# Optimization experiments

Hardware: AMD Instinct MI355X
Metric: run time of the kernel (lower is better)

Reference implementation:

```python
import jax, jax.numpy as jnp
import numpy as np

MAX_THRESHOLD = 0.95


def leaky_clamp(x, lo, hi, slope):
    # identity inside [lo, hi], linear with `slope` outside
    return jnp.where(x < lo, lo + slope * (x - lo),
                     jnp.where(x > hi, hi + slope * (x - hi), x))


def or_gate_layer(x, W, tau_adder):
    # x: (B, in), W: (out, in)
    in_f = W.shape[1]
    tau_floor = float(np.log(in_f - 1) + np.log(MAX_THRESHOLD) - np.log(1.0 - MAX_THRESHOLD))
    tau = tau_floor + jax.nn.leaky_relu(tau_adder, negative_slope=0.05)
    aw = leaky_clamp(W, 0.0, 1.0, 0.1)           # (out, in)
    z = x[:, None, :] * aw[None, :, :]           # (B, out, in) broadcast
    p = jax.nn.softmax(tau * z, axis=-1)         # tau-scaled softmax over in
    return jnp.sum(p * z, axis=-1)               # (B, out)


def setup_inputs() -> dict:
    key = jax.random.key(0)
    ks = jax.random.split(key, 9)
    input_dim = 512
    layer_dims = [1024, 512, 256, 128]
    x = jax.random.uniform(ks[0], (128, input_dim), dtype=jnp.float32)
    in_dim = input_dim * 2
    out = {"x": x}
    for i, out_dim in enumerate(layer_dims):
        out[f"W{i}"] = jax.random.normal(ks[1 + i], (out_dim, in_dim), dtype=jnp.float32)
        out[f"tau{i}"] = jnp.zeros((), dtype=jnp.float32)
        in_dim = out_dim  # only_inverter=True
    return out


def reference(x, W0, W1, W2, W3, tau0, tau1, tau2, tau3):
    h = jnp.concatenate([x, 1.0 - x], axis=-1)   # pass_invert
    for W, t in ((W0, tau0), (W1, tau1), (W2, tau2), (W3, tau3)):
        h = 1.0 - or_gate_layer(h, W, t)         # only_inverter: invert after every layer
    return h
```

## Files before the change

### kernel.cpp

```cpp
#include <hip/hip_runtime.h>
#include <math.h>

#if defined(__has_builtin)
#  if __has_builtin(__builtin_amdgcn_exp2f)
#    define EXP2F(x) __builtin_amdgcn_exp2f(x)
#  endif
#endif
#ifndef EXP2F
#  define EXP2F(x) __expf(0.69314718055994530942f * (x))
#endif

__device__ __forceinline__ float fast_exp2(float x) {
  const float M = 12582912.0f;
  const float y = x + M;
  const float n = y - M;
  const float f = x - n;
  float p = fmaf(f, 0.055504109f, 0.24022651f);
  p = fmaf(f, p, 0.69314718f);
  p = fmaf(f, p, 1.0f);
  const int r = (__float_as_int(y) << 23) + __float_as_int(p);
  return __int_as_float(r);
}

template <int IN, int OUT, int BB, bool FIRST>
__launch_bounds__(256, 4)
__global__ void or_layer(const float* __restrict__ hin,
                         const float* __restrict__ W,
                         const float* __restrict__ tau_ptr,
                         float* __restrict__ hout,
                         float tau_floor) {
  constexpr int OBB = 2;
  constexpr int NIT = IN / 64;
  constexpr int nOT = OUT / 32;
  constexpr int IN4 = IN / 4;

  __shared__ float4 lds_h[BB][IN4];

  const int tid  = threadIdx.x;
  const int lane = tid & 63;
  const int wid  = tid >> 6;
  const int il   = lane & 15;
  const int og   = lane >> 4;

  const int ot = blockIdx.x % nOT;
  const int bt = blockIdx.x / nOT;
  const int b0 = bt * BB;
  const int o0 = ot * 32 + wid * 8 + og * OBB;

  const float ta  = tau_ptr[0];
  const float tau = tau_floor + (ta >= 0.0f ? ta : 0.05f * ta);
  const float c2  = tau * 1.44269504088896340736f;

  const float4* __restrict__ Wv = (const float4*)W;
  const float4* __restrict__ Hv = (const float4*)hin;

  if (FIRST) {
    constexpr int HALF4 = IN / 8;
    for (int idx = tid; idx < BB * HALF4; idx += 256) {
      const int r = idx / HALF4;
      const int k = idx - r * HALF4;
      const float4 v = Hv[(b0 + r) * HALF4 + k];
      lds_h[r][k] = v;
      lds_h[r][HALF4 + k] =
          make_float4(1.0f - v.x, 1.0f - v.y, 1.0f - v.z, 1.0f - v.w);
    }
  } else {
    for (int idx = tid; idx < BB * IN4; idx += 256) {
      const int r = idx / IN4;
      const int k = idx - r * IN4;
      lds_h[r][k] = Hv[(b0 + r) * IN4 + k];
    }
  }
  __syncthreads();

  float s[BB][OBB], t[BB][OBB];
#pragma unroll
  for (int r = 0; r < BB; ++r)
#pragma unroll
    for (int c = 0; c < OBB; ++c) { s[r][c] = 0.0f; t[r][c] = 0.0f; }

  const float4* wp0 = Wv + (size_t)(o0 + 0) * IN4 + il;
  const float4* wp1 = Wv + (size_t)(o0 + 1) * IN4 + il;

  float4 wcur0 = wp0[0];
  float4 wcur1 = wp1[0];

#pragma unroll 2
  for (int ic = 0; ic < NIT; ++ic) {
    const int icn = (ic + 1 < NIT) ? (ic + 1) : (NIT - 1);
    const float4 wnxt0 = wp0[icn * 16];
    const float4 wnxt1 = wp1[icn * 16];

    float hc[BB][4];
#pragma unroll
    for (int r = 0; r < BB; ++r) {
      const float4 v = lds_h[r][ic * 16 + il];
      hc[r][0] = v.x; hc[r][1] = v.y; hc[r][2] = v.z; hc[r][3] = v.w;
    }

    float cw[OBB][4];
    {
      const float wj0[4] = {wcur0.x, wcur0.y, wcur0.z, wcur0.w};
      const float wj1[4] = {wcur1.x, wcur1.y, wcur1.z, wcur1.w};
#pragma unroll
      for (int j = 0; j < 4; ++j) {
        float m  = fminf(fmaxf(wj0[j], 0.0f), 1.0f);
        cw[0][j] = c2 * fmaf(0.1f, wj0[j] - m, m);
        m        = fminf(fmaxf(wj1[j], 0.0f), 1.0f);
        cw[1][j] = c2 * fmaf(0.1f, wj1[j] - m, m);
      }
    }

#pragma unroll
    for (int r = 0; r < BB; ++r)
#pragma unroll
      for (int c = 0; c < OBB; ++c)
#pragma unroll
        for (int j = 0; j < 4; ++j) {
          const float arg = cw[c][j] * hc[r][j];
          const float e = (j & 1) ? fast_exp2(arg) : EXP2F(arg);
          s[r][c] += e;
          t[r][c]  = fmaf(arg, e, t[r][c]);
        }

    wcur0 = wnxt0;
    wcur1 = wnxt1;
  }

#pragma unroll
  for (int m = 1; m < 16; m <<= 1)
#pragma unroll
    for (int r = 0; r < BB; ++r)
#pragma unroll
      for (int c = 0; c < OBB; ++c) {
        s[r][c] += __shfl_xor(s[r][c], m, 64);
        t[r][c] += __shfl_xor(t[r][c], m, 64);
      }

  if (il == 0) {
    const float inv_c2 = 1.0f / c2;
#pragma unroll
    for (int r = 0; r < BB; ++r)
#pragma unroll
      for (int c = 0; c < OBB; ++c) {
        const float out = t[r][c] / s[r][c] * inv_c2;
        hout[(b0 + r) * OUT + (o0 + c)] = 1.0f - out;
      }
  }
}

extern "C" void kernel_launch(void* const* d_in, const int* in_sizes, int n_in,
                              void* d_out, int out_size, void* d_ws, size_t ws_size,
                              hipStream_t stream) {
  const float* x    = (const float*)d_in[0];
  const float* W0   = (const float*)d_in[1];
  const float* tau0 = (const float*)d_in[2];
  const float* W1   = (const float*)d_in[3];
  const float* tau1 = (const float*)d_in[4];
  const float* W2   = (const float*)d_in[5];
  const float* tau2 = (const float*)d_in[6];
  const float* W3   = (const float*)d_in[7];
  const float* tau3 = (const float*)d_in[8];

  float* h1  = (float*)d_ws;
  float* h2  = h1 + 128 * 1024;
  float* h3  = h2 + 128 * 512;
  float* out = (float*)d_out;

  const double LOGR = 2.9444389791664403;
  const float tf1024 = (float)(log(1023.0) + LOGR);
  const float tf512  = (float)(log(511.0)  + LOGR);
  const float tf256  = (float)(log(255.0)  + LOGR);

  or_layer<1024, 1024, 4, true ><<<1024, 256, 0, stream>>>(x,  W0, tau0, h1,  tf1024);
  or_layer<1024,  512, 2, false><<<1024, 256, 0, stream>>>(h1, W1, tau1, h2,  tf1024);
  or_layer< 512,  256, 1, false><<<1024, 256, 0, stream>>>(h2, W2, tau2, h3,  tf512);
  or_layer< 256,  128, 1, false><<< 512, 256, 0, stream>>>(h3, W3, tau3, out, tf256);
}
```

Before: 123.8 us.

## Fuse four OR-gate layers into one persistent cooperative kernel with grid syncs

Replaces four separate layer launches with a single cooperative persistent kernel. It loops over tiles per layer and puts grid-wide syncs between layers, with a fallback to the separate launches if the cooperative launch fails. This targets launch overhead and the tail gaps between dependent kernels. In exchange it adds grid barrier costs and grid-stride tile scheduling. It also uses a fixed 16KB shared buffer sized for the largest layer, which may lower occupancy for the smaller layers.

```diff
diff --git a/kernel.cpp b/kernel.cpp
--- a/kernel.cpp
+++ b/kernel.cpp
@@ -1,5 +1,8 @@
 #include <hip/hip_runtime.h>
+#include <hip/hip_cooperative_groups.h>
 #include <math.h>
+
+namespace cg = cooperative_groups;
 
 #if defined(__has_builtin)
 #  if __has_builtin(__builtin_amdgcn_exp2f)
@@ -23,130 +26,166 @@
 }
 
 template <int IN, int OUT, int BB, bool FIRST>
+__device__ __forceinline__ void layer_body(const float* __restrict__ hin,
+                                           const float* __restrict__ W,
+                                           const float* __restrict__ tau_ptr,
+                                           float* __restrict__ hout,
+                                           float tau_floor,
+                                           float4* __restrict__ lds_h) {
+  constexpr int OBB = 2;
+  constexpr int NIT = IN / 64;
+  constexpr int nOT = OUT / 32;
+  constexpr int IN4 = IN / 4;
+  constexpr int TILES = nOT * (128 / BB);
+
+  const int tid  = threadIdx.x;
+  const int lane = tid & 63;
+  const int wid  = tid >> 6;
+  const int il   = lane & 15;
+  const int og   = lane >> 4;
+
+  const float ta  = tau_ptr[0];
+  const float tau = tau_floor + (ta >= 0.0f ? ta : 0.05f * ta);
+  const float c2  = tau * 1.44269504088896340736f;
+  const float inv_c2 = 1.0f / c2;
+
+  const float4* __restrict__ Wv = (const float4*)W;
+  const float4* __restrict__ Hv = (const float4*)hin;
+
+  for (int tile = blockIdx.x; tile < TILES; tile += gridDim.x) {
+    const int ot = tile % nOT;
+    const int bt = tile / nOT;
+    const int b0 = bt * BB;
+    const int o0 = ot * 32 + wid * 8 + og * OBB;
+
+    __syncthreads();
+    if (FIRST) {
+      constexpr int HALF4 = IN / 8;
+      for (int idx = tid; idx < BB * HALF4; idx += 256) {
+        const int r = idx / HALF4;
+        const int k = idx - r * HALF4;
+        const float4 v = Hv[(b0 + r) * HALF4 + k];
+        lds_h[r * IN4 + k] = v;
+        lds_h[r * IN4 + HALF4 + k] =
+            make_float4(1.0f - v.x, 1.0f - v.y, 1.0f - v.z, 1.0f - v.w);
+      }
+    } else {
+      for (int idx = tid; idx < BB * IN4; idx += 256) {
+        const int r = idx / IN4;
+        const int k = idx - r * IN4;
+        lds_h[r * IN4 + k] = Hv[(b0 + r) * IN4 + k];
+      }
+    }
+    __syncthreads();
+
+    float s[BB][OBB], t[BB][OBB];
+#pragma unroll
+    for (int r = 0; r < BB; ++r)
+#pragma unroll
+      for (int c = 0; c < OBB; ++c) { s[r][c] = 0.0f; t[r][c] = 0.0f; }
+
+    const float4* wp0 = Wv + (size_t)(o0 + 0) * IN4 + il;
+    const float4* wp1 = Wv + (size_t)(o0 + 1) * IN4 + il;
+    float4 wcur0 = wp0[0];
+    float4 wcur1 = wp1[0];
+
+#pragma unroll 2
+    for (int ic = 0; ic < NIT; ++ic) {
+      const int icn = (ic + 1 < NIT) ? (ic + 1) : (NIT - 1);
+      const float4 wnxt0 = wp0[icn * 16];
+      const float4 wnxt1 = wp1[icn * 16];
+
+      float hc[BB][4];
+#pragma unroll
+      for (int r = 0; r < BB; ++r) {
+        const float4 v = lds_h[r * IN4 + ic * 16 + il];
+        hc[r][0] = v.x; hc[r][1] = v.y; hc[r][2] = v.z; hc[r][3] = v.w;
+      }
+
+      float cw[OBB][4];
+      {
+        const float wj0[4] = {wcur0.x, wcur0.y, wcur0.z, wcur0.w};
+        const float wj1[4] = {wcur1.x, wcur1.y, wcur1.z, wcur1.w};
+#pragma unroll
+        for (int j = 0; j < 4; ++j) {
+          float m  = fminf(fmaxf(wj0[j], 0.0f), 1.0f);
+          cw[0][j] = c2 * fmaf(0.1f, wj0[j] - m, m);
+          m        = fminf(fmaxf(wj1[j], 0.0f), 1.0f);
+          cw[1][j] = c2 * fmaf(0.1f, wj1[j] - m, m);
+        }
+      }
+
+#pragma unroll
+      for (int r = 0; r < BB; ++r)
+#pragma unroll
+        for (int c = 0; c < OBB; ++c)
+#pragma unroll
+          for (int j = 0; j < 4; ++j) {
+            const float arg = cw[c][j] * hc[r][j];
+            const float e = (j & 1) ? fast_exp2(arg) : EXP2F(arg);
+            s[r][c] += e;
+            t[r][c]  = fmaf(arg, e, t[r][c]);
+          }
+
+      wcur0 = wnxt0;
+      wcur1 = wnxt1;
+    }
+
+#pragma unroll
+    for (int m = 1; m < 16; m <<= 1)
+#pragma unroll
+      for (int r = 0; r < BB; ++r)
+#pragma unroll
+        for (int c = 0; c < OBB; ++c) {
+          s[r][c] += __shfl_xor(s[r][c], m, 64);
+          t[r][c] += __shfl_xor(t[r][c], m, 64);
+        }
+
+    if (il == 0) {
+#pragma unroll
+      for (int r = 0; r < BB; ++r)
+#pragma unroll
+        for (int c = 0; c < OBB; ++c) {
+          const float out = t[r][c] / s[r][c] * inv_c2;
+          hout[(b0 + r) * OUT + (o0 + c)] = 1.0f - out;
+        }
+    }
+  }
+}
+
+__launch_bounds__(256, 4)
+__global__ void fused_net(const float* __restrict__ x,
+                          const float* __restrict__ W0, const float* __restrict__ tau0,
+                          const float* __restrict__ W1, const float* __restrict__ tau1,
+                          const float* __restrict__ W2, const float* __restrict__ tau2,
+                          const float* __restrict__ W3, const float* __restrict__ tau3,
+                          float* __restrict__ h1, float* __restrict__ h2,
+                          float* __restrict__ h3, float* __restrict__ out,
+                          float tf0, float tf1, float tf2, float tf3) {
+  __shared__ float4 lds_h[1024];
+  cg::grid_group grid = cg::this_grid();
+
+  layer_body<1024, 1024, 4, true >(x,  W0, tau0, h1,  tf0, lds_h);
+  __threadfence();
+  grid.sync();
+  layer_body<1024,  512, 2, false>(h1, W1, tau1, h2,  tf1, lds_h);
+  __threadfence();
+  grid.sync();
+  layer_body< 512,  256, 1, false>(h2, W2, tau2, h3,  tf2, lds_h);
+  __threadfence();
+  grid.sync();
+  layer_body< 256,  128, 1, false>(h3, W3, tau3, out, tf3, lds_h);
+}
+
+template <int IN, int OUT, int BB, bool FIRST>
 __launch_bounds__(256, 4)
 __global__ void or_layer(const float* __restrict__ hin,
                          const float* __restrict__ W,
                          const float* __restrict__ tau_ptr,
                          float* __restrict__ hout,
                          float tau_floor) {
-  constexpr int OBB = 2;
-  constexpr int NIT = IN / 64;
-  constexpr int nOT = OUT / 32;
-  constexpr int IN4 = IN / 4;
-
-  __shared__ float4 lds_h[BB][IN4];
-
-  const int tid  = threadIdx.x;
-  const int lane = tid & 63;
-  const int wid  = tid >> 6;
-  const int il   = lane & 15;
-  const int og   = lane >> 4;
-
-  const int ot = blockIdx.x % nOT;
-  const int bt = blockIdx.x / nOT;
-  const int b0 = bt * BB;
-  const int o0 = ot * 32 + wid * 8 + og * OBB;
-
-  const float ta  = tau_ptr[0];
-  const float tau = tau_floor + (ta >= 0.0f ? ta : 0.05f * ta);
-  const float c2  = tau * 1.44269504088896340736f;
-
-  const float4* __restrict__ Wv = (const float4*)W;
-  const float4* __restrict__ Hv = (const float4*)hin;
-
-  if (FIRST) {
-    constexpr int HALF4 = IN / 8;
-    for (int idx = tid; idx < BB * HALF4; idx += 256) {
-      const int r = idx / HALF4;
-      const int k = idx - r * HALF4;
-      const float4 v = Hv[(b0 + r) * HALF4 + k];
-      lds_h[r][k] = v;
-      lds_h[r][HALF4 + k] =
-          make_float4(1.0f - v.x, 1.0f - v.y, 1.0f - v.z, 1.0f - v.w);
-    }
-  } else {
-    for (int idx = tid; idx < BB * IN4; idx += 256) {
-      const int r = idx / IN4;
-      const int k = idx - r * IN4;
-      lds_h[r][k] = Hv[(b0 + r) * IN4 + k];
-    }
-  }
-  __syncthreads();
-
-  float s[BB][OBB], t[BB][OBB];
-#pragma unroll
-  for (int r = 0; r < BB; ++r)
-#pragma unroll
-    for (int c = 0; c < OBB; ++c) { s[r][c] = 0.0f; t[r][c] = 0.0f; }
-
-  const float4* wp0 = Wv + (size_t)(o0 + 0) * IN4 + il;
-  const float4* wp1 = Wv + (size_t)(o0 + 1) * IN4 + il;
-
-  float4 wcur0 = wp0[0];
-  float4 wcur1 = wp1[0];
-
-#pragma unroll 2
-  for (int ic = 0; ic < NIT; ++ic) {
-    const int icn = (ic + 1 < NIT) ? (ic + 1) : (NIT - 1);
-    const float4 wnxt0 = wp0[icn * 16];
-    const float4 wnxt1 = wp1[icn * 16];
-
-    float hc[BB][4];
-#pragma unroll
-    for (int r = 0; r < BB; ++r) {
-      const float4 v = lds_h[r][ic * 16 + il];
-      hc[r][0] = v.x; hc[r][1] = v.y; hc[r][2] = v.z; hc[r][3] = v.w;
-    }
-
-    float cw[OBB][4];
-    {
-      const float wj0[4] = {wcur0.x, wcur0.y, wcur0.z, wcur0.w};
-      const float wj1[4] = {wcur1.x, wcur1.y, wcur1.z, wcur1.w};
-#pragma unroll
-      for (int j = 0; j < 4; ++j) {
-        float m  = fminf(fmaxf(wj0[j], 0.0f), 1.0f);
-        cw[0][j] = c2 * fmaf(0.1f, wj0[j] - m, m);
-        m        = fminf(fmaxf(wj1[j], 0.0f), 1.0f);
-        cw[1][j] = c2 * fmaf(0.1f, wj1[j] - m, m);
-      }
-    }
-
-#pragma unroll
-    for (int r = 0; r < BB; ++r)
-#pragma unroll
-      for (int c = 0; c < OBB; ++c)
-#pragma unroll
-        for (int j = 0; j < 4; ++j) {
-          const float arg = cw[c][j] * hc[r][j];
-          const float e = (j & 1) ? fast_exp2(arg) : EXP2F(arg);
-          s[r][c] += e;
-          t[r][c]  = fmaf(arg, e, t[r][c]);
-        }
-
-    wcur0 = wnxt0;
-    wcur1 = wnxt1;
-  }
-
-#pragma unroll
-  for (int m = 1; m < 16; m <<= 1)
-#pragma unroll
-    for (int r = 0; r < BB; ++r)
-#pragma unroll
-      for (int c = 0; c < OBB; ++c) {
-        s[r][c] += __shfl_xor(s[r][c], m, 64);
-        t[r][c] += __shfl_xor(t[r][c], m, 64);
-      }
-
-  if (il == 0) {
-    const float inv_c2 = 1.0f / c2;
-#pragma unroll
-    for (int r = 0; r < BB; ++r)
-#pragma unroll
-      for (int c = 0; c < OBB; ++c) {
-        const float out = t[r][c] / s[r][c] * inv_c2;
-        hout[(b0 + r) * OUT + (o0 + c)] = 1.0f - out;
-      }
-  }
+  __shared__ float4 lds_h[(BB * IN) / 4];
+  layer_body<IN, OUT, BB, FIRST>(hin, W, tau_ptr, hout, tau_floor, lds_h);
 }
 
 extern "C" void kernel_launch(void* const* d_in, const int* in_sizes, int n_in,
@@ -168,12 +207,29 @@
   float* out = (float*)d_out;
 
   const double LOGR = 2.9444389791664403;
-  const float tf1024 = (float)(log(1023.0) + LOGR);
-  const float tf512  = (float)(log(511.0)  + LOGR);
-  const float tf256  = (float)(log(255.0)  + LOGR);
-
-  or_layer<1024, 1024, 4, true ><<<1024, 256, 0, stream>>>(x,  W0, tau0, h1,  tf1024);
-  or_layer<1024,  512, 2, false><<<1024, 256, 0, stream>>>(h1, W1, tau1, h2,  tf1024);
-  or_layer< 512,  256, 1, false><<<1024, 256, 0, stream>>>(h2, W2, tau2, h3,  tf512);
-  or_layer< 256,  128, 1, false><<< 512, 256, 0, stream>>>(h3, W3, tau3, out, tf256);
-}
+  float tf1024 = (float)(log(1023.0) + LOGR);
+  float tf512  = (float)(log(511.0)  + LOGR);
+  float tf256  = (float)(log(255.0)  + LOGR);
+
+  static int nblk = 0;
+  if (nblk == 0) {
+    int per_cu = 0;
+    if (hipOccupancyMaxActiveBlocksPerMultiprocessor(&per_cu, fused_net, 256, 0)
+            != hipSuccess || per_cu <= 0)
+      per_cu = 1;
+    nblk = per_cu * 256;
+    if (nblk > 1024) nblk = 1024;
+  }
+
+  void* args[] = {&x,  &W0, &tau0, &W1, &tau1, &W2, &tau2, &W3, &tau3,
+                  &h1, &h2, &h3,   &out, &tf1024, &tf1024, &tf512, &tf256};
+  hipError_t err = hipLaunchCooperativeKernel(
+      fused_net, dim3(nblk), dim3(256), args, 0, stream);
+
+  if (err != hipSuccess) {
+    or_layer<1024, 1024, 4, true ><<<1024, 256, 0, stream>>>(x,  W0, tau0, h1,  tf1024);
+    or_layer<1024,  512, 2, false><<<1024, 256, 0, stream>>>(h1, W1, tau1, h2,  tf1024);
+    or_layer< 512,  256, 1, false><<<1024, 256, 0, stream>>>(h2, W2, tau2, h3,  tf512);
+    or_layer< 256,  128, 1, false><<< 512, 256, 0, stream>>>(h3, W3, tau3, out, tf256);
+  }
+}
```

Result: slower. 437.3 us (+253.4%).

## Fuse last three OR layers into one per-row kernel with LDS intermediates

Applied to the files above, without the earlier changes.

Replaces the three separate launches for layers 1 to 3 with one kernel. Each 1024-thread block handles one batch row and keeps the intermediate activations in shared memory between layers. This removes two kernel launches and the global round trips for h2 and h3. In exchange, only 128 blocks run, fewer than the 256 CUs on the device. There is also no batch reuse of weights, so every block streams all of W1, W2 and W3 from cache, and the weight loads are no longer software-prefetched.

```diff
diff --git a/kernel.cpp b/kernel.cpp
--- a/kernel.cpp
+++ b/kernel.cpp
@@ -21,6 +21,7 @@
   const int r = (__float_as_int(y) << 23) + __float_as_int(p);
   return __int_as_float(r);
 }
+
 
 template <int IN, int OUT, int BB, bool FIRST>
 __launch_bounds__(256, 4)
@@ -34,7 +35,7 @@
   constexpr int nOT = OUT / 32;
   constexpr int IN4 = IN / 4;
 
-  __shared__ float4 lds_h[BB][IN4];
+  __shared__ float4 lds_h[BB * IN4];
 
   const int tid  = threadIdx.x;
   const int lane = tid & 63;
@@ -60,15 +61,15 @@
       const int r = idx / HALF4;
       const int k = idx - r * HALF4;
       const float4 v = Hv[(b0 + r) * HALF4 + k];
-      lds_h[r][k] = v;
-      lds_h[r][HALF4 + k] =
+      lds_h[r * IN4 + k] = v;
+      lds_h[r * IN4 + HALF4 + k] =
           make_float4(1.0f - v.x, 1.0f - v.y, 1.0f - v.z, 1.0f - v.w);
     }
   } else {
     for (int idx = tid; idx < BB * IN4; idx += 256) {
       const int r = idx / IN4;
       const int k = idx - r * IN4;
-      lds_h[r][k] = Hv[(b0 + r) * IN4 + k];
+      lds_h[r * IN4 + k] = Hv[(b0 + r) * IN4 + k];
     }
   }
   __syncthreads();
@@ -81,7 +82,6 @@
 
   const float4* wp0 = Wv + (size_t)(o0 + 0) * IN4 + il;
   const float4* wp1 = Wv + (size_t)(o0 + 1) * IN4 + il;
-
   float4 wcur0 = wp0[0];
   float4 wcur1 = wp1[0];
 
@@ -94,7 +94,7 @@
     float hc[BB][4];
 #pragma unroll
     for (int r = 0; r < BB; ++r) {
-      const float4 v = lds_h[r][ic * 16 + il];
+      const float4 v = lds_h[r * IN4 + ic * 16 + il];
       hc[r][0] = v.x; hc[r][1] = v.y; hc[r][2] = v.z; hc[r][3] = v.w;
     }
 
@@ -147,6 +147,95 @@
         hout[(b0 + r) * OUT + (o0 + c)] = 1.0f - out;
       }
   }
+}
+
+template <int IN, int OUT, bool LAST>
+__device__ __forceinline__ void sub_layer(const float4* __restrict__ in4,
+                                          const float* __restrict__ W,
+                                          const float* __restrict__ tau_ptr,
+                                          float tau_floor,
+                                          float* __restrict__ out_lds,
+                                          float* __restrict__ out_glob) {
+  constexpr int NIT = IN / 64;
+  constexpr int IN4 = IN / 4;
+  constexpr int OPG = OUT / 64;
+
+  const int tid = threadIdx.x;
+  const int il  = tid & 15;
+  const int g   = tid >> 4;
+
+  const float ta  = tau_ptr[0];
+  const float tau = tau_floor + (ta >= 0.0f ? ta : 0.05f * ta);
+  const float c2  = tau * 1.44269504088896340736f;
+  const float inv_c2 = 1.0f / c2;
+
+  const float4* __restrict__ Wv = (const float4*)W;
+
+#pragma unroll
+  for (int ob = 0; ob < OPG / 2; ++ob) {
+    const int o0 = g * OPG + ob * 2;
+    float s0 = 0.0f, s1 = 0.0f, t0 = 0.0f, t1 = 0.0f;
+
+#pragma unroll 2
+    for (int ic = 0; ic < NIT; ++ic) {
+      const float4 hv = in4[ic * 16 + il];
+      const float4 w0 = Wv[(size_t)(o0 + 0) * IN4 + ic * 16 + il];
+      const float4 w1 = Wv[(size_t)(o0 + 1) * IN4 + ic * 16 + il];
+      const float h[4] = {hv.x, hv.y, hv.z, hv.w};
+      const float a[4] = {w0.x, w0.y, w0.z, w0.w};
+      const float b[4] = {w1.x, w1.y, w1.z, w1.w};
+#pragma unroll
+      for (int j = 0; j < 4; ++j) {
+        float m = fminf(fmaxf(a[j], 0.0f), 1.0f);
+        const float ca = c2 * fmaf(0.1f, a[j] - m, m);
+        m = fminf(fmaxf(b[j], 0.0f), 1.0f);
+        const float cb = c2 * fmaf(0.1f, b[j] - m, m);
+        const float arga = ca * h[j];
+        const float argb = cb * h[j];
+        const float ea = (j & 1) ? fast_exp2(arga) : EXP2F(arga);
+        const float eb = (j & 1) ? fast_exp2(argb) : EXP2F(argb);
+        s0 += ea; t0 = fmaf(arga, ea, t0);
+        s1 += eb; t1 = fmaf(argb, eb, t1);
+      }
+    }
+
+#pragma unroll
+    for (int m = 1; m < 16; m <<= 1) {
+      s0 += __shfl_xor(s0, m, 64); t0 += __shfl_xor(t0, m, 64);
+      s1 += __shfl_xor(s1, m, 64); t1 += __shfl_xor(t1, m, 64);
+    }
+
+    if (il == 0) {
+      const float r0 = 1.0f - t0 / s0 * inv_c2;
+      const float r1 = 1.0f - t1 / s1 * inv_c2;
+      if (LAST) { out_glob[o0] = r0; out_glob[o0 + 1] = r1; }
+      else      { out_lds[o0]  = r0; out_lds[o0 + 1]  = r1; }
+    }
+  }
+}
+
+__launch_bounds__(1024)
+__global__ void fused_tail(const float* __restrict__ h1,
+                           const float* __restrict__ W1, const float* __restrict__ tau1,
+                           const float* __restrict__ W2, const float* __restrict__ tau2,
+                           const float* __restrict__ W3, const float* __restrict__ tau3,
+                           float* __restrict__ out,
+                           float tf_a, float tf_b, float tf_c) {
+  __shared__ float4 hA[256];
+  __shared__ float4 hB[128];
+  __shared__ float4 hC[64];
+
+  const int row = blockIdx.x;
+  const int tid = threadIdx.x;
+
+  if (tid < 256) hA[tid] = ((const float4*)h1)[row * 256 + tid];
+  __syncthreads();
+
+  sub_layer<1024, 512, false>(hA, W1, tau1, tf_a, (float*)hB, nullptr);
+  __syncthreads();
+  sub_layer< 512, 256, false>(hB, W2, tau2, tf_b, (float*)hC, nullptr);
+  __syncthreads();
+  sub_layer< 256, 128, true >(hC, W3, tau3, tf_c, nullptr, out + row * 128);
 }
 
 extern "C" void kernel_launch(void* const* d_in, const int* in_sizes, int n_in,
@@ -163,8 +252,6 @@
   const float* tau3 = (const float*)d_in[8];
 
   float* h1  = (float*)d_ws;
-  float* h2  = h1 + 128 * 1024;
-  float* h3  = h2 + 128 * 512;
   float* out = (float*)d_out;
 
   const double LOGR = 2.9444389791664403;
@@ -172,8 +259,7 @@
   const float tf512  = (float)(log(511.0)  + LOGR);
   const float tf256  = (float)(log(255.0)  + LOGR);
 
-  or_layer<1024, 1024, 4, true ><<<1024, 256, 0, stream>>>(x,  W0, tau0, h1,  tf1024);
-  or_layer<1024,  512, 2, false><<<1024, 256, 0, stream>>>(h1, W1, tau1, h2,  tf1024);
-  or_layer< 512,  256, 1, false><<<1024, 256, 0, stream>>>(h2, W2, tau2, h3,  tf512);
-  or_layer< 256,  128, 1, false><<< 512, 256, 0, stream>>>(h3, W3, tau3, out, tf256);
-}
+  or_layer<1024, 1024, 4, true><<<1024, 256, 0, stream>>>(x, W0, tau0, h1, tf1024);
+  fused_tail<<<128, 1024, 0, stream>>>(h1, W1, tau1, W2, tau2, W3, tau3,
+                                       out, tf1024, tf512, tf256);
+}
```

After: 148.4 us. 1.2x slower.
